# Kernel tuning notes

Measured on AMD Instinct MI355X. Metric: run time of the kernel, lower is better.

Reference implementation:

```python
import jax, jax.numpy as jnp
import numpy as np

B, H, N, D, R, HIDDEN = 4, 12, 1025, 64, 1, 32


def _make_tables(N, R):
    # Geometry tables, mirroring FlexAttentionCPB.init_tables
    P = N - R
    S = int(P ** 0.5)
    assert S * S == P
    rng = np.arange(-(S - 1), S, dtype=np.float32)        # [2S-1]
    dY, dX = np.meshgrid(rng, rng, indexing='ij')
    rel = np.stack([dY / max(S - 1, 1), dX / max(S - 1, 1)], axis=-1).reshape(-1, 2)
    rel_table = np.sign(rel) * np.log1p(np.abs(rel))      # [(2S-1)^2, 2]
    yy = np.arange(S)
    Y, X = np.meshgrid(yy, yy, indexing='ij')
    flat = np.stack([Y, X], 0).reshape(2, -1)             # [2, P]
    d = (flat[:, :, None] - flat[:, None, :]).transpose(1, 2, 0).copy()  # [P,P,2]
    d[:, :, 0] += S - 1
    d[:, :, 1] += S - 1
    d[:, :, 0] *= 2 * S - 1
    l_idx = d.sum(-1).astype(np.int32)
    idx = np.full((N, N), -1, dtype=np.int32)
    idx[R:, R:] = l_idx
    return jnp.asarray(rel_table, jnp.float32), jnp.asarray(idx)


def setup_inputs() -> dict:
    key = jax.random.key(0)
    ks = jax.random.split(key, 8)
    rel_table, idx_table = _make_tables(N, R)
    return {
        'q': jax.random.normal(ks[0], (B, H, N, D), jnp.float32),
        'k': jax.random.normal(ks[1], (B, H, N, D), jnp.float32),
        'v': jax.random.normal(ks[2], (B, H, N, D), jnp.float32),
        'mu': jax.random.normal(ks[3], (B, H, 2, N), jnp.float32),
        'w1': jax.random.normal(ks[4], (2, HIDDEN), jnp.float32) * 0.5,
        'b1': jax.random.normal(ks[5], (HIDDEN,), jnp.float32) * 0.05,
        'w2': jax.random.normal(ks[6], (HIDDEN, H), jnp.float32) * 0.1,
        'gamma': jnp.zeros((H,), jnp.float32),   # nn.Parameter(torch.zeros(H))
        'rel_table': rel_table,
        'idx_table': idx_table,
    }


def reference(q, k, v, mu, w1, b1, w2, gamma, rel_table, idx_table):
    d = q.shape[-1]
    # CPB MLP: Linear(2,hidden)+GELU(exact)+Linear(hidden,H,no bias) -> [L,H]
    bt = jax.nn.gelu(rel_table @ w1 + b1, approximate=False) @ w2
    has_bias = (idx_table >= 0)                       # [N,N] == (q>=R)&(kv>=R)
    idx_c = jnp.where(has_bias, idx_table, 0)
    bias = jnp.transpose(bt[idx_c], (2, 0, 1))        # [H,N,N]
    mu_q = mu[:, :, 0, :]                             # [B,H,N]
    mu_k = mu[:, :, 1, :]
    gate = jax.nn.sigmoid(gamma)[None, :, None, None] * (
        mu_q[..., :, None] + mu_k[..., None, :])      # [B,H,N,N]
    scale = 1.0 / jnp.sqrt(jnp.asarray(d, q.dtype))
    scores = jnp.einsum('bhqd,bhkd->bhqk', q, k) * scale
    scores = scores + has_bias[None, None].astype(scores.dtype) * gate * bias[None]
    attn = jax.nn.softmax(scores, axis=-1)
    return jnp.einsum('bhqk,bhkd->bhqd', attn, v)
```

## Files before the change

kernel.cpp:

```cpp
#include <hip/hip_runtime.h>
#include <math.h>

#define B_ 4
#define H_ 12
#define N_ 1025
#define D_ 64
#define HID_ 32
#define TBL_ 3969
#define NQT 17
#define NBLK (B_ * H_ * NQT)
#define LOG2E 1.44269504f
#define THR_ 12.0f

typedef _Float16 half8 __attribute__((ext_vector_type(8)));
typedef __fp16 fp16x2 __attribute__((ext_vector_type(2)));
typedef float f32x4 __attribute__((ext_vector_type(4)));
typedef float f32x4u __attribute__((ext_vector_type(4), aligned(4)));

#if defined(__has_builtin)
#if __has_builtin(__builtin_amdgcn_exp2f)
#define EX2 __builtin_amdgcn_exp2f
#else
#define EX2 exp2f
#endif
#else
#define EX2 exp2f
#endif

#define AKT_OFF 0
#define BTR_OFF 208896
#define KF_OFF 399408
#define VF_OFF 7084080

__device__ __forceinline__ void stage16(const _Float16* gsrc, _Float16* ldst) {
    __builtin_amdgcn_global_load_lds(
        (const __attribute__((address_space(1))) void*)gsrc,
        (__attribute__((address_space(3))) void*)ldst, 16, 0, 0);
}

__global__ __launch_bounds__(256) void prep(
    const float* __restrict__ K, const float* __restrict__ V,
    const float* __restrict__ MU, const float* __restrict__ GAMMA,
    const float* __restrict__ rel, const float* __restrict__ w1,
    const float* __restrict__ b1, const float* __restrict__ w2,
    _Float16* __restrict__ Kf, _Float16* __restrict__ Vf,
    float* __restrict__ akT, float* __restrict__ btR) {
    const int bid = blockIdx.x;
    const int tid = threadIdx.x;
    if (bid < NBLK) {
        __shared__ float Vls[64 * 65];
        __shared__ __align__(16) float Kls[64 * 64];
        const int bh = bid / NQT, kt = bid % NQT;
        const size_t base = (size_t)bh * (N_ * D_);
        const int k0 = kt * 64;
#pragma unroll
        for (int it = 0; it < 4; ++it) {
            const int idx = it * 256 + tid;
            const int kr = idx >> 4, c4 = (idx & 15) << 2;
            const int kg = k0 + kr;
            float4 v4 = make_float4(0, 0, 0, 0), k4 = v4;
            if (kg < N_) {
                v4 = *(const float4*)(V + base + (size_t)kg * D_ + c4);
                k4 = *(const float4*)(K + base + (size_t)kg * D_ + c4);
            }
            Vls[(c4 + 0) * 65 + kr] = v4.x;
            Vls[(c4 + 1) * 65 + kr] = v4.y;
            Vls[(c4 + 2) * 65 + kr] = v4.z;
            Vls[(c4 + 3) * 65 + kr] = v4.w;
            const int gi = (c4 >> 2) ^ (kr & 15);
            *(float4*)&Kls[kr * 64 + (gi << 2)] = k4;
        }
        if (tid < 64) {
            const int kk = k0 + tid;
            const int h = bh % H_;
            const float sgl = LOG2E / (1.f + __expf(-GAMMA[h]));
            float a = 0.f;
            if (kk >= 1 && kk < N_) a = sgl * MU[((size_t)bh * 2 + 1) * N_ + kk];
            akT[bh * 1088 + kk] = a;
        }
        __syncthreads();
        const int lane = tid & 63, lq = lane & 15, g = lane >> 4;
        const int fbh = tid >> 6;
        const size_t tb = (size_t)(bh * NQT + kt) * 4096;
#pragma unroll
        for (int x = 0; x < 2; ++x) {
            const int fb = fbh + x * 4;
            {
                const int kh = fb >> 2, dg = fb & 3;
                const float* vp = &Vls[(dg * 16 + lq) * 65 + kh * 32 + g * 8];
                half8 v8;
#pragma unroll
                for (int j = 0; j < 8; ++j) v8[j] = (_Float16)vp[j];
                *(half8*)&Vf[tb + fb * 512 + lane * 8] = v8;
            }
            {
                const int row = (fb >> 1) * 16 + lq;
                const int col = (fb & 1) * 32 + g * 8;
                const int ga = ((col >> 2) + 0) ^ (row & 15);
                const int gb = ((col >> 2) + 1) ^ (row & 15);
                f32x4 a = *(const f32x4*)&Kls[row * 64 + (ga << 2)];
                f32x4 b = *(const f32x4*)&Kls[row * 64 + (gb << 2)];
                half8 k8;
                k8[0] = (_Float16)a[0]; k8[1] = (_Float16)a[1];
                k8[2] = (_Float16)a[2]; k8[3] = (_Float16)a[3];
                k8[4] = (_Float16)b[0]; k8[5] = (_Float16)b[1];
                k8[6] = (_Float16)b[2]; k8[7] = (_Float16)b[3];
                *(half8*)&Kf[tb + fb * 512 + lane * 8] = k8;
            }
        }
    } else {
        const int i = (bid - NBLK) * 256 + tid;
        if (i < TBL_) {
            const float x0 = rel[2 * i + 0], x1 = rel[2 * i + 1];
            float acc[H_];
#pragma unroll
            for (int h = 0; h < H_; ++h) acc[h] = 0.f;
#pragma unroll
            for (int j = 0; j < HID_; ++j) {
                float t = fmaf(x0, w1[j], fmaf(x1, w1[HID_ + j], b1[j]));
                float gl = 0.5f * t * (1.f + erff(t * 0.7071067811865475f));
#pragma unroll
                for (int h = 0; h < H_; ++h) acc[h] = fmaf(gl, w2[j * H_ + h], acc[h]);
            }
#pragma unroll
            for (int h = 0; h < H_; ++h) btR[h * TBL_ + (TBL_ - 1 - i)] = acc[h];
        }
    }
}

__global__ __launch_bounds__(256, 4) void flex_attn(
    const float* __restrict__ Q, const _Float16* __restrict__ Kf,
    const _Float16* __restrict__ Vf, const float* __restrict__ MU,
    const float* __restrict__ GAMMA, const char* __restrict__ btb,
    const float* __restrict__ akT, float* __restrict__ OUT) {
    __shared__ __align__(16) _Float16 Ks[2][4096];
    __shared__ __align__(16) _Float16 Vs[2][4096];

    const int bid = blockIdx.x;
    const int swz0 = (bid & 7) * (NBLK / 8) + (bid >> 3);
    const int bh = swz0 / NQT;
    const int qt = swz0 % NQT;
    const int h = bh % H_;
    const int tid = threadIdx.x;
    const int w = tid >> 6;
    const int lane = tid & 63;
    const int lq = lane & 15;
    const int g = lane >> 4;

    const size_t base = (size_t)bh * (N_ * D_);
    const float sg = LOG2E / (1.f + __expf(-GAMMA[h]));

    const int qrow = qt * 64 + w * 16 + lq;
    const bool qv = qrow < N_;

    half8 qf[2];
#pragma unroll
    for (int dh = 0; dh < 2; ++dh) {
        float4 t0 = make_float4(0, 0, 0, 0), t1 = t0;
        if (qv) {
            const float4* qp = (const float4*)(Q + base + (size_t)qrow * D_ + dh * 32 + g * 8);
            t0 = qp[0]; t1 = qp[1];
        }
        const float qs = 0.125f * LOG2E;
        half8 q8;
        q8[0] = (_Float16)(t0.x * qs); q8[1] = (_Float16)(t0.y * qs);
        q8[2] = (_Float16)(t0.z * qs); q8[3] = (_Float16)(t0.w * qs);
        q8[4] = (_Float16)(t1.x * qs); q8[5] = (_Float16)(t1.y * qs);
        q8[6] = (_Float16)(t1.z * qs); q8[7] = (_Float16)(t1.w * qs);
        qf[dh] = q8;
    }

    const bool qb = qv && (qrow >= 1);
    const float qbf = qb ? 1.f : 0.f;
    float aq = 0.f;
    int cq = 0;
    if (qb) {
        const int pq = qrow - 1;
        cq = (pq >> 5) * 63 + (pq & 31);
        aq = sg * MU[(size_t)bh * 2 * N_ + qrow];
    }
    int boff4[4];
#pragma unroll
    for (int kg = 0; kg < 4; ++kg) {
        const int pk0 = kg * 16 + g * 4 - 1;
        const int ck0 = (pk0 >> 5) * 63 + (pk0 & 31);
        boff4[kg] = (h * TBL_ + 1984 - cq + ck0) * 4;
    }
    const float* akb = akT + bh * 1088;
    const _Float16* kfb = Kf + (size_t)bh * NQT * 4096;
    const _Float16* vfb = Vf + (size_t)bh * NQT * 4096;

    f32x4 o[4];
    const f32x4 zz = {0.f, 0.f, 0.f, 0.f};
#pragma unroll
    for (int dg = 0; dg < 4; ++dg) o[dg] = zz;
    float m = 0.f, lsum = 0.f;

    stage16(kfb + (2 * w + 0) * 512 + lane * 8, &Ks[0][(2 * w + 0) * 512]);
    stage16(kfb + (2 * w + 1) * 512 + lane * 8, &Ks[0][(2 * w + 1) * 512]);
    stage16(vfb + (2 * w + 0) * 512 + lane * 8, &Vs[0][(2 * w + 0) * 512]);
    stage16(vfb + (2 * w + 1) * 512 + lane * 8, &Vs[0][(2 * w + 1) * 512]);
    __syncthreads();

    const int pswz = (lq & 7) << 4;

    for (int t = 0; t < NQT; ++t) {
        const int buf = t & 1;
        const int kt0 = t * 64;
        char* plw = (char*)&Ks[buf][0] + w * 2048;

        float bt16[16];
#pragma unroll
        for (int kg = 0; kg < 4; ++kg) {
            const int off = boff4[kg];
            if (kg & 1) {
                f32x4u f4 = *(const f32x4u*)(btb + off);
                bt16[kg * 4 + 0] = f4[0];
                bt16[kg * 4 + 1] = f4[1];
                bt16[kg * 4 + 2] = f4[2];
                bt16[kg * 4 + 3] = f4[3];
            } else {
                const bool cross = (g == 0);
                f32x4u f4 = *(const f32x4u*)(btb + off + (cross ? 128 : 0));
                const float s0v = *(const float*)(btb + off);
                bt16[kg * 4 + 0] = s0v;
                bt16[kg * 4 + 1] = cross ? f4[0] : f4[1];
                bt16[kg * 4 + 2] = cross ? f4[1] : f4[2];
                bt16[kg * 4 + 3] = cross ? f4[2] : f4[3];
            }
            boff4[kg] += 504;
        }
        f32x4 akq[4];
#pragma unroll
        for (int kg = 0; kg < 4; ++kg)
            akq[kg] = *(const f32x4*)(akb + kt0 + kg * 16 + g * 4);

        if (t + 1 < NQT) {
            const _Float16* kn = kfb + (size_t)(t + 1) * 4096;
            const _Float16* vn = vfb + (size_t)(t + 1) * 4096;
            stage16(kn + (2 * w + 0) * 512 + lane * 8, &Ks[buf ^ 1][(2 * w + 0) * 512]);
            stage16(kn + (2 * w + 1) * 512 + lane * 8, &Ks[buf ^ 1][(2 * w + 1) * 512]);
            stage16(vn + (2 * w + 0) * 512 + lane * 8, &Vs[buf ^ 1][(2 * w + 0) * 512]);
            stage16(vn + (2 * w + 1) * 512 + lane * 8, &Vs[buf ^ 1][(2 * w + 1) * 512]);
        }

        const _Float16* ksl = &Ks[buf][lane * 8];
        f32x4 sa[4];
#pragma unroll
        for (int kg = 0; kg < 4; ++kg) {
            half8 a0 = *(const half8*)(ksl + (2 * kg + 0) * 512);
            half8 a1 = *(const half8*)(ksl + (2 * kg + 1) * 512);
            f32x4 z = zz;
            z = __builtin_amdgcn_mfma_f32_16x16x32_f16(a0, qf[0], z, 0, 0, 0);
            z = __builtin_amdgcn_mfma_f32_16x16x32_f16(a1, qf[1], z, 0, 0, 0);
            sa[kg] = z;
        }
        asm volatile("s_waitcnt lgkmcnt(0)" ::: "memory");
        __builtin_amdgcn_s_barrier();
        __builtin_amdgcn_sched_barrier(0);

        if (t == 0 && g == 0) bt16[0] = 0.f;
        float s[16];
#pragma unroll
        for (int kg = 0; kg < 4; ++kg) {
#pragma unroll
            for (int r = 0; r < 4; ++r) {
                const int i = kg * 4 + r;
                s[i] = fmaf(fmaf(qbf, akq[kg][r], aq), bt16[i], sa[kg][r]);
            }
        }
        if (t == NQT - 1) {
#pragma unroll
            for (int kg = 0; kg < 4; ++kg)
#pragma unroll
                for (int r = 0; r < 4; ++r) {
                    const int i = kg * 4 + r;
                    if (1024 + kg * 16 + g * 4 + r >= N_) s[i] = -1e30f;
                }
        }

        float lmax = s[0];
#pragma unroll
        for (int i = 1; i < 16; ++i) lmax = fmaxf(lmax, s[i]);
        if (t == 0) {
            float mt = fmaxf(lmax, __shfl_xor(lmax, 16));
            m = fmaxf(mt, __shfl_xor(mt, 32));
        } else if (!__all(lmax <= m + THR_)) {
            float mt = fmaxf(lmax, __shfl_xor(lmax, 16));
            mt = fmaxf(mt, __shfl_xor(mt, 32));
            const float mnew = fmaxf(m, mt);
            const float cc = EX2(m - mnew);
            m = mnew;
            lsum *= cc;
            float cc4[4];
#pragma unroll
            for (int r = 0; r < 4; ++r) cc4[r] = __shfl(cc, g * 4 + r);
#pragma unroll
            for (int dg = 0; dg < 4; ++dg)
#pragma unroll
                for (int r = 0; r < 4; ++r) o[dg][r] *= cc4[r];
        }
        float pv16[16];
        float ls0 = 0.f, ls1 = 0.f;
#pragma unroll
        for (int i = 0; i < 16; i += 2) {
            pv16[i] = EX2(s[i] - m);
            pv16[i + 1] = EX2(s[i + 1] - m);
            ls0 += pv16[i];
            ls1 += pv16[i + 1];
        }
        lsum += ls0 + ls1;

#pragma unroll
        for (int kg = 0; kg < 4; ++kg) {
            fp16x2 h0 = __builtin_amdgcn_cvt_pkrtz(pv16[kg * 4 + 0], pv16[kg * 4 + 1]);
            fp16x2 h1 = __builtin_amdgcn_cvt_pkrtz(pv16[kg * 4 + 2], pv16[kg * 4 + 3]);
            uint2 u = make_uint2(__builtin_bit_cast(uint32_t, h0),
                                 __builtin_bit_cast(uint32_t, h1));
            *(uint2*)(plw + lq * 128 + ((kg * 32 + g * 8) ^ pswz)) = u;
        }

#pragma unroll
        for (int kh = 0; kh < 2; ++kh) {
            half8 pa = *(const half8*)(plw + lq * 128 + ((kh * 64 + g * 16) ^ pswz));
#pragma unroll
            for (int dg = 0; dg < 4; ++dg) {
                half8 vb8 = *(const half8*)&Vs[buf][(kh * 4 + dg) * 512 + lane * 8];
                o[dg] = __builtin_amdgcn_mfma_f32_16x16x32_f16(pa, vb8, o[dg], 0, 0, 0);
            }
        }
        __syncthreads();
    }

    lsum += __shfl_xor(lsum, 16);
    lsum += __shfl_xor(lsum, 32);
    const float linv = 1.f / lsum;
    float li4[4];
#pragma unroll
    for (int r = 0; r < 4; ++r) li4[r] = __shfl(linv, g * 4 + r);
#pragma unroll
    for (int dg = 0; dg < 4; ++dg) {
#pragma unroll
        for (int r = 0; r < 4; ++r) {
            const int qq = qt * 64 + w * 16 + g * 4 + r;
            if (qq < N_) OUT[base + (size_t)qq * D_ + dg * 16 + lq] = o[dg][r] * li4[r];
        }
    }
}

extern "C" void kernel_launch(void* const* d_in, const int* in_sizes, int n_in,
                              void* d_out, int out_size, void* d_ws, size_t ws_size,
                              hipStream_t stream) {
    const float* q = (const float*)d_in[0];
    const float* k = (const float*)d_in[1];
    const float* v = (const float*)d_in[2];
    const float* mu = (const float*)d_in[3];
    const float* w1 = (const float*)d_in[4];
    const float* b1 = (const float*)d_in[5];
    const float* w2 = (const float*)d_in[6];
    const float* gamma = (const float*)d_in[7];
    const float* rel = (const float*)d_in[8];

    char* ws = (char*)d_ws;
    float* akT = (float*)(ws + AKT_OFF);
    float* btR = (float*)(ws + BTR_OFF);
    _Float16* Kf = (_Float16*)(ws + KF_OFF);
    _Float16* Vf = (_Float16*)(ws + VF_OFF);

    prep<<<NBLK + (TBL_ + 255) / 256, 256, 0, stream>>>(k, v, mu, gamma, rel, w1, b1, w2,
                                                        Kf, Vf, akT, btR);
    flex_attn<<<NBLK, 256, 0, stream>>>(q, Kf, Vf, mu, gamma, ws + BTR_OFF, akT,
                                        (float*)d_out);
}
```

Measured before the change: 61.41 us.

## Split KV range across two blocks per query tile with merge kernel

```diff
diff --git a/kernel.cpp b/kernel.cpp
--- a/kernel.cpp
+++ b/kernel.cpp
@@ -9,6 +9,7 @@
 #define TBL_ 3969
 #define NQT 17
 #define NBLK (B_ * H_ * NQT)
+#define NBLK2 (NBLK * 2)
 #define LOG2E 1.44269504f
 #define THR_ 12.0f
 
@@ -31,6 +32,9 @@
 #define BTR_OFF 208896
 #define KF_OFF 399408
 #define VF_OFF 7084080
+#define OP_OFF 13768768
+#define ML_OFF 27138112
+#define WS_NEED 27973696ull
 
 __device__ __forceinline__ void stage16(const _Float16* gsrc, _Float16* ldst) {
     __builtin_amdgcn_global_load_lds(
@@ -128,18 +132,34 @@
     }
 }
 
+template <int SPLIT>
 __global__ __launch_bounds__(256, 4) void flex_attn(
     const float* __restrict__ Q, const _Float16* __restrict__ Kf,
     const _Float16* __restrict__ Vf, const float* __restrict__ MU,
     const float* __restrict__ GAMMA, const char* __restrict__ btb,
-    const float* __restrict__ akT, float* __restrict__ OUT) {
+    const float* __restrict__ akT, _Float16* __restrict__ Opart,
+    float* __restrict__ mlb, float* __restrict__ OUT) {
     __shared__ __align__(16) _Float16 Ks[2][4096];
     __shared__ __align__(16) _Float16 Vs[2][4096];
 
     const int bid = blockIdx.x;
-    const int swz0 = (bid & 7) * (NBLK / 8) + (bid >> 3);
-    const int bh = swz0 / NQT;
-    const int qt = swz0 % NQT;
+    int bh, qt, kh, tstart, tend;
+    if (SPLIT) {
+        const int swz0 = (bid & 7) * (NBLK2 / 8) + (bid >> 3);
+        bh = swz0 / (NQT * 2);
+        const int rr = swz0 % (NQT * 2);
+        qt = rr >> 1;
+        kh = rr & 1;
+        tstart = kh ? 9 : 0;
+        tend = kh ? NQT : 9;
+    } else {
+        const int swz0 = (bid & 7) * (NBLK / 8) + (bid >> 3);
+        bh = swz0 / NQT;
+        qt = swz0 % NQT;
+        kh = 0;
+        tstart = 0;
+        tend = NQT;
+    }
     const int h = bh % H_;
     const int tid = threadIdx.x;
     const int w = tid >> 6;
@@ -184,7 +204,7 @@
     for (int kg = 0; kg < 4; ++kg) {
         const int pk0 = kg * 16 + g * 4 - 1;
         const int ck0 = (pk0 >> 5) * 63 + (pk0 & 31);
-        boff4[kg] = (h * TBL_ + 1984 - cq + ck0) * 4;
+        boff4[kg] = (h * TBL_ + 1984 - cq + ck0) * 4 + tstart * 504;
     }
     const float* akb = akT + bh * 1088;
     const _Float16* kfb = Kf + (size_t)bh * NQT * 4096;
@@ -196,15 +216,21 @@
     for (int dg = 0; dg < 4; ++dg) o[dg] = zz;
     float m = 0.f, lsum = 0.f;
 
-    stage16(kfb + (2 * w + 0) * 512 + lane * 8, &Ks[0][(2 * w + 0) * 512]);
-    stage16(kfb + (2 * w + 1) * 512 + lane * 8, &Ks[0][(2 * w + 1) * 512]);
-    stage16(vfb + (2 * w + 0) * 512 + lane * 8, &Vs[0][(2 * w + 0) * 512]);
-    stage16(vfb + (2 * w + 1) * 512 + lane * 8, &Vs[0][(2 * w + 1) * 512]);
+    {
+        const _Float16* kp = kfb + (size_t)tstart * 4096;
+        const _Float16* vp = vfb + (size_t)tstart * 4096;
+        _Float16* kd = &Ks[tstart & 1][0];
+        _Float16* vd = &Vs[tstart & 1][0];
+        stage16(kp + (2 * w + 0) * 512 + lane * 8, kd + (2 * w + 0) * 512);
+        stage16(kp + (2 * w + 1) * 512 + lane * 8, kd + (2 * w + 1) * 512);
+        stage16(vp + (2 * w + 0) * 512 + lane * 8, vd + (2 * w + 0) * 512);
+        stage16(vp + (2 * w + 1) * 512 + lane * 8, vd + (2 * w + 1) * 512);
+    }
     __syncthreads();
 
     const int pswz = (lq & 7) << 4;
 
-    for (int t = 0; t < NQT; ++t) {
+    for (int t = tstart; t < tend; ++t) {
         const int buf = t & 1;
         const int kt0 = t * 64;
         char* plw = (char*)&Ks[buf][0] + w * 2048;
@@ -235,7 +261,7 @@
         for (int kg = 0; kg < 4; ++kg)
             akq[kg] = *(const f32x4*)(akb + kt0 + kg * 16 + g * 4);
 
-        if (t + 1 < NQT) {
+        if (t + 1 < tend) {
             const _Float16* kn = kfb + (size_t)(t + 1) * 4096;
             const _Float16* vn = vfb + (size_t)(t + 1) * 4096;
             stage16(kn + (2 * w + 0) * 512 + lane * 8, &Ks[buf ^ 1][(2 * w + 0) * 512]);
@@ -282,7 +308,7 @@
         float lmax = s[0];
 #pragma unroll
         for (int i = 1; i < 16; ++i) lmax = fmaxf(lmax, s[i]);
-        if (t == 0) {
+        if (t == tstart) {
             float mt = fmaxf(lmax, __shfl_xor(lmax, 16));
             m = fmaxf(mt, __shfl_xor(mt, 32));
         } else if (!__all(lmax <= m + THR_)) {
@@ -321,11 +347,11 @@
         }
 
 #pragma unroll
-        for (int kh = 0; kh < 2; ++kh) {
-            half8 pa = *(const half8*)(plw + lq * 128 + ((kh * 64 + g * 16) ^ pswz));
+        for (int khx = 0; khx < 2; ++khx) {
+            half8 pa = *(const half8*)(plw + lq * 128 + ((khx * 64 + g * 16) ^ pswz));
 #pragma unroll
             for (int dg = 0; dg < 4; ++dg) {
-                half8 vb8 = *(const half8*)&Vs[buf][(kh * 4 + dg) * 512 + lane * 8];
+                half8 vb8 = *(const half8*)&Vs[buf][(khx * 4 + dg) * 512 + lane * 8];
                 o[dg] = __builtin_amdgcn_mfma_f32_16x16x32_f16(pa, vb8, o[dg], 0, 0, 0);
             }
         }
@@ -338,14 +364,64 @@
     float li4[4];
 #pragma unroll
     for (int r = 0; r < 4; ++r) li4[r] = __shfl(linv, g * 4 + r);
-#pragma unroll
-    for (int dg = 0; dg < 4; ++dg) {
-#pragma unroll
-        for (int r = 0; r < 4; ++r) {
-            const int qq = qt * 64 + w * 16 + g * 4 + r;
-            if (qq < N_) OUT[base + (size_t)qq * D_ + dg * 16 + lq] = o[dg][r] * li4[r];
-        }
-    }
+    if (SPLIT) {
+        _Float16* op = Opart + (size_t)(bh * 2 + kh) * (1088 * 64);
+#pragma unroll
+        for (int dg = 0; dg < 4; ++dg) {
+#pragma unroll
+            for (int r = 0; r < 4; ++r) {
+                const int qq = qt * 64 + w * 16 + g * 4 + r;
+                op[(size_t)qq * 64 + dg * 16 + lq] = (_Float16)(o[dg][r] * li4[r]);
+            }
+        }
+        if (g == 0 && qv) {
+            float2* mlp = (float2*)mlb + (size_t)(bh * 2 + kh) * 1088 + qrow;
+            *mlp = make_float2(m, lsum);
+        }
+    } else {
+#pragma unroll
+        for (int dg = 0; dg < 4; ++dg) {
+#pragma unroll
+            for (int r = 0; r < 4; ++r) {
+                const int qq = qt * 64 + w * 16 + g * 4 + r;
+                if (qq < N_) OUT[base + (size_t)qq * D_ + dg * 16 + lq] = o[dg][r] * li4[r];
+            }
+        }
+    }
+}
+
+__global__ __launch_bounds__(256) void merge(const _Float16* __restrict__ Opart,
+                                             const float* __restrict__ mlb,
+                                             float* __restrict__ OUT) {
+    const int idx = blockIdx.x * 256 + threadIdx.x;
+    if (idx >= B_ * H_ * N_ * 8) return;
+    const int d8 = (idx & 7) * 8;
+    const int rg = idx >> 3;
+    const int bh = rg / N_;
+    const int qq = rg % N_;
+    const float2 ml0 = ((const float2*)mlb)[(size_t)(bh * 2 + 0) * 1088 + qq];
+    const float2 ml1 = ((const float2*)mlb)[(size_t)(bh * 2 + 1) * 1088 + qq];
+    const float M = fmaxf(ml0.x, ml1.x);
+    const float w0 = ml0.y * EX2(ml0.x - M);
+    const float w1 = ml1.y * EX2(ml1.x - M);
+    const float inv = 1.f / (w0 + w1);
+    const float c0 = w0 * inv, c1 = w1 * inv;
+    const half8 o0 = *(const half8*)(Opart + (size_t)(bh * 2 + 0) * (1088 * 64) +
+                                     (size_t)qq * 64 + d8);
+    const half8 o1 = *(const half8*)(Opart + (size_t)(bh * 2 + 1) * (1088 * 64) +
+                                     (size_t)qq * 64 + d8);
+    float* op = OUT + (size_t)bh * (N_ * D_) + (size_t)qq * 64 + d8;
+    float4 r0, r1;
+    r0.x = fmaf(c0, (float)o0[0], c1 * (float)o1[0]);
+    r0.y = fmaf(c0, (float)o0[1], c1 * (float)o1[1]);
+    r0.z = fmaf(c0, (float)o0[2], c1 * (float)o1[2]);
+    r0.w = fmaf(c0, (float)o0[3], c1 * (float)o1[3]);
+    r1.x = fmaf(c0, (float)o0[4], c1 * (float)o1[4]);
+    r1.y = fmaf(c0, (float)o0[5], c1 * (float)o1[5]);
+    r1.z = fmaf(c0, (float)o0[6], c1 * (float)o1[6]);
+    r1.w = fmaf(c0, (float)o0[7], c1 * (float)o1[7]);
+    ((float4*)op)[0] = r0;
+    ((float4*)op)[1] = r1;
 }
 
 extern "C" void kernel_launch(void* const* d_in, const int* in_sizes, int n_in,
@@ -366,9 +442,18 @@
     float* btR = (float*)(ws + BTR_OFF);
     _Float16* Kf = (_Float16*)(ws + KF_OFF);
     _Float16* Vf = (_Float16*)(ws + VF_OFF);
+    _Float16* Opart = (_Float16*)(ws + OP_OFF);
+    float* mlb = (float*)(ws + ML_OFF);
 
     prep<<<NBLK + (TBL_ + 255) / 256, 256, 0, stream>>>(k, v, mu, gamma, rel, w1, b1, w2,
                                                         Kf, Vf, akT, btR);
-    flex_attn<<<NBLK, 256, 0, stream>>>(q, Kf, Vf, mu, gamma, ws + BTR_OFF, akT,
-                                        (float*)d_out);
+    if (ws_size >= WS_NEED) {
+        flex_attn<1><<<NBLK2, 256, 0, stream>>>(q, Kf, Vf, mu, gamma, ws + BTR_OFF, akT,
+                                                Opart, mlb, (float*)d_out);
+        merge<<<(B_ * H_ * N_ * 8 + 255) / 256, 256, 0, stream>>>(Opart, mlb,
+                                                                  (float*)d_out);
+    } else {
+        flex_attn<0><<<NBLK, 256, 0, stream>>>(q, Kf, Vf, mu, gamma, ws + BTR_OFF, akT,
+                                               Opart, mlb, (float*)d_out);
+    }
 }
```

New measurement: 65.50 us. 6.6% more time.

## Split KV tile across warp pairs, each warp handling two query groups with LDS merge

Applied to the files above, without the earlier changes.

```diff
diff --git a/kernel.cpp b/kernel.cpp
--- a/kernel.cpp
+++ b/kernel.cpp
@@ -128,7 +128,7 @@
     }
 }
 
-__global__ __launch_bounds__(256, 4) void flex_attn(
+__global__ __launch_bounds__(256, 3) void flex_attn(
     const float* __restrict__ Q, const _Float16* __restrict__ Kf,
     const _Float16* __restrict__ Vf, const float* __restrict__ MU,
     const float* __restrict__ GAMMA, const char* __restrict__ btb,
@@ -143,6 +143,8 @@
     const int h = bh % H_;
     const int tid = threadIdx.x;
     const int w = tid >> 6;
+    const int kh = w & 1;
+    const int qh = w >> 1;
     const int lane = tid & 63;
     const int lq = lane & 15;
     const int g = lane >> 4;
@@ -150,51 +152,61 @@
     const size_t base = (size_t)bh * (N_ * D_);
     const float sg = LOG2E / (1.f + __expf(-GAMMA[h]));
 
-    const int qrow = qt * 64 + w * 16 + lq;
-    const bool qv = qrow < N_;
-
-    half8 qf[2];
-#pragma unroll
-    for (int dh = 0; dh < 2; ++dh) {
-        float4 t0 = make_float4(0, 0, 0, 0), t1 = t0;
-        if (qv) {
-            const float4* qp = (const float4*)(Q + base + (size_t)qrow * D_ + dh * 32 + g * 8);
-            t0 = qp[0]; t1 = qp[1];
-        }
-        const float qs = 0.125f * LOG2E;
-        half8 q8;
-        q8[0] = (_Float16)(t0.x * qs); q8[1] = (_Float16)(t0.y * qs);
-        q8[2] = (_Float16)(t0.z * qs); q8[3] = (_Float16)(t0.w * qs);
-        q8[4] = (_Float16)(t1.x * qs); q8[5] = (_Float16)(t1.y * qs);
-        q8[6] = (_Float16)(t1.z * qs); q8[7] = (_Float16)(t1.w * qs);
-        qf[dh] = q8;
-    }
-
-    const bool qb = qv && (qrow >= 1);
-    const float qbf = qb ? 1.f : 0.f;
-    float aq = 0.f;
-    int cq = 0;
-    if (qb) {
-        const int pq = qrow - 1;
-        cq = (pq >> 5) * 63 + (pq & 31);
-        aq = sg * MU[(size_t)bh * 2 * N_ + qrow];
-    }
-    int boff4[4];
-#pragma unroll
-    for (int kg = 0; kg < 4; ++kg) {
-        const int pk0 = kg * 16 + g * 4 - 1;
-        const int ck0 = (pk0 >> 5) * 63 + (pk0 & 31);
-        boff4[kg] = (h * TBL_ + 1984 - cq + ck0) * 4;
+    half8 qf[2][2];
+    bool qb[2];
+    float aq[2], qbf[2];
+    int cq[2];
+#pragma unroll
+    for (int qg = 0; qg < 2; ++qg) {
+        const int qrow = qt * 64 + qh * 32 + qg * 16 + lq;
+        const bool qv = qrow < N_;
+#pragma unroll
+        for (int dh = 0; dh < 2; ++dh) {
+            float4 t0 = make_float4(0, 0, 0, 0), t1 = t0;
+            if (qv) {
+                const float4* qp =
+                    (const float4*)(Q + base + (size_t)qrow * D_ + dh * 32 + g * 8);
+                t0 = qp[0]; t1 = qp[1];
+            }
+            const float qs = 0.125f * LOG2E;
+            half8 q8;
+            q8[0] = (_Float16)(t0.x * qs); q8[1] = (_Float16)(t0.y * qs);
+            q8[2] = (_Float16)(t0.z * qs); q8[3] = (_Float16)(t0.w * qs);
+            q8[4] = (_Float16)(t1.x * qs); q8[5] = (_Float16)(t1.y * qs);
+            q8[6] = (_Float16)(t1.z * qs); q8[7] = (_Float16)(t1.w * qs);
+            qf[qg][dh] = q8;
+        }
+        qb[qg] = qv && (qrow >= 1);
+        qbf[qg] = qb[qg] ? 1.f : 0.f;
+        aq[qg] = 0.f;
+        cq[qg] = 0;
+        if (qb[qg]) {
+            const int pq = qrow - 1;
+            cq[qg] = (pq >> 5) * 63 + (pq & 31);
+            aq[qg] = sg * MU[(size_t)bh * 2 * N_ + qrow];
+        }
+    }
+    int boff4[2][2];
+#pragma unroll
+    for (int qg = 0; qg < 2; ++qg) {
+#pragma unroll
+        for (int kg = 0; kg < 2; ++kg) {
+            const int pk0 = kh * 32 + kg * 16 + g * 4 - 1;
+            const int ck0 = (pk0 >> 5) * 63 + (pk0 & 31);
+            boff4[qg][kg] = (h * TBL_ + 1984 - cq[qg] + ck0) * 4;
+        }
     }
     const float* akb = akT + bh * 1088;
     const _Float16* kfb = Kf + (size_t)bh * NQT * 4096;
     const _Float16* vfb = Vf + (size_t)bh * NQT * 4096;
 
-    f32x4 o[4];
+    f32x4 o[2][4];
     const f32x4 zz = {0.f, 0.f, 0.f, 0.f};
 #pragma unroll
-    for (int dg = 0; dg < 4; ++dg) o[dg] = zz;
-    float m = 0.f, lsum = 0.f;
+    for (int qg = 0; qg < 2; ++qg)
+#pragma unroll
+        for (int dg = 0; dg < 4; ++dg) o[qg][dg] = zz;
+    float m[2] = {0.f, 0.f}, lsum[2] = {0.f, 0.f};
 
     stage16(kfb + (2 * w + 0) * 512 + lane * 8, &Ks[0][(2 * w + 0) * 512]);
     stage16(kfb + (2 * w + 1) * 512 + lane * 8, &Ks[0][(2 * w + 1) * 512]);
@@ -202,38 +214,39 @@
     stage16(vfb + (2 * w + 1) * 512 + lane * 8, &Vs[0][(2 * w + 1) * 512]);
     __syncthreads();
 
-    const int pswz = (lq & 7) << 4;
+    const int pswz = (lq & 3) << 4;
 
     for (int t = 0; t < NQT; ++t) {
         const int buf = t & 1;
         const int kt0 = t * 64;
         char* plw = (char*)&Ks[buf][0] + w * 2048;
 
-        float bt16[16];
-#pragma unroll
-        for (int kg = 0; kg < 4; ++kg) {
-            const int off = boff4[kg];
-            if (kg & 1) {
-                f32x4u f4 = *(const f32x4u*)(btb + off);
-                bt16[kg * 4 + 0] = f4[0];
-                bt16[kg * 4 + 1] = f4[1];
-                bt16[kg * 4 + 2] = f4[2];
-                bt16[kg * 4 + 3] = f4[3];
-            } else {
-                const bool cross = (g == 0);
-                f32x4u f4 = *(const f32x4u*)(btb + off + (cross ? 128 : 0));
-                const float s0v = *(const float*)(btb + off);
-                bt16[kg * 4 + 0] = s0v;
-                bt16[kg * 4 + 1] = cross ? f4[0] : f4[1];
-                bt16[kg * 4 + 2] = cross ? f4[1] : f4[2];
-                bt16[kg * 4 + 3] = cross ? f4[2] : f4[3];
-            }
-            boff4[kg] += 504;
-        }
-        f32x4 akq[4];
-#pragma unroll
-        for (int kg = 0; kg < 4; ++kg)
-            akq[kg] = *(const f32x4*)(akb + kt0 + kg * 16 + g * 4);
+        float bt[2][8];
+#pragma unroll
+        for (int qg = 0; qg < 2; ++qg) {
+#pragma unroll
+            for (int kg = 0; kg < 2; ++kg) {
+                const int off = boff4[qg][kg];
+                if (kg == 1) {
+                    f32x4u f4 = *(const f32x4u*)(btb + off);
+                    bt[qg][4] = f4[0]; bt[qg][5] = f4[1];
+                    bt[qg][6] = f4[2]; bt[qg][7] = f4[3];
+                } else {
+                    const bool cross = (g == 0);
+                    f32x4u f4 = *(const f32x4u*)(btb + off + (cross ? 128 : 0));
+                    const float s0v = *(const float*)(btb + off);
+                    bt[qg][0] = s0v;
+                    bt[qg][1] = cross ? f4[0] : f4[1];
+                    bt[qg][2] = cross ? f4[1] : f4[2];
+                    bt[qg][3] = cross ? f4[2] : f4[3];
+                }
+                boff4[qg][kg] += 504;
+            }
+        }
+        f32x4 akq[2];
+#pragma unroll
+        for (int kg = 0; kg < 2; ++kg)
+            akq[kg] = *(const f32x4*)(akb + kt0 + kh * 32 + kg * 16 + g * 4);
 
         if (t + 1 < NQT) {
             const _Float16* kn = kfb + (size_t)(t + 1) * 4096;
@@ -244,106 +257,146 @@
             stage16(vn + (2 * w + 1) * 512 + lane * 8, &Vs[buf ^ 1][(2 * w + 1) * 512]);
         }
 
-        const _Float16* ksl = &Ks[buf][lane * 8];
-        f32x4 sa[4];
-#pragma unroll
-        for (int kg = 0; kg < 4; ++kg) {
+        const _Float16* ksl = &Ks[buf][kh * 2048 + lane * 8];
+        f32x4 sa[2][2];
+#pragma unroll
+        for (int kg = 0; kg < 2; ++kg) {
             half8 a0 = *(const half8*)(ksl + (2 * kg + 0) * 512);
             half8 a1 = *(const half8*)(ksl + (2 * kg + 1) * 512);
-            f32x4 z = zz;
-            z = __builtin_amdgcn_mfma_f32_16x16x32_f16(a0, qf[0], z, 0, 0, 0);
-            z = __builtin_amdgcn_mfma_f32_16x16x32_f16(a1, qf[1], z, 0, 0, 0);
-            sa[kg] = z;
+#pragma unroll
+            for (int qg = 0; qg < 2; ++qg) {
+                f32x4 z = zz;
+                z = __builtin_amdgcn_mfma_f32_16x16x32_f16(a0, qf[qg][0], z, 0, 0, 0);
+                z = __builtin_amdgcn_mfma_f32_16x16x32_f16(a1, qf[qg][1], z, 0, 0, 0);
+                sa[qg][kg] = z;
+            }
         }
         asm volatile("s_waitcnt lgkmcnt(0)" ::: "memory");
         __builtin_amdgcn_s_barrier();
         __builtin_amdgcn_sched_barrier(0);
 
-        if (t == 0 && g == 0) bt16[0] = 0.f;
-        float s[16];
-#pragma unroll
-        for (int kg = 0; kg < 4; ++kg) {
-#pragma unroll
-            for (int r = 0; r < 4; ++r) {
-                const int i = kg * 4 + r;
-                s[i] = fmaf(fmaf(qbf, akq[kg][r], aq), bt16[i], sa[kg][r]);
-            }
-        }
-        if (t == NQT - 1) {
-#pragma unroll
-            for (int kg = 0; kg < 4; ++kg)
+        if (t == 0 && kh == 0 && g == 0) { bt[0][0] = 0.f; bt[1][0] = 0.f; }
+#pragma unroll
+        for (int qg = 0; qg < 2; ++qg) {
+            float s[8];
+#pragma unroll
+            for (int kg = 0; kg < 2; ++kg)
 #pragma unroll
                 for (int r = 0; r < 4; ++r) {
                     const int i = kg * 4 + r;
-                    if (1024 + kg * 16 + g * 4 + r >= N_) s[i] = -1e30f;
+                    s[i] = fmaf(fmaf(qbf[qg], akq[kg][r], aq[qg]), bt[qg][i],
+                                sa[qg][kg][r]);
                 }
-        }
-
-        float lmax = s[0];
-#pragma unroll
-        for (int i = 1; i < 16; ++i) lmax = fmaxf(lmax, s[i]);
-        if (t == 0) {
-            float mt = fmaxf(lmax, __shfl_xor(lmax, 16));
-            m = fmaxf(mt, __shfl_xor(mt, 32));
-        } else if (!__all(lmax <= m + THR_)) {
-            float mt = fmaxf(lmax, __shfl_xor(lmax, 16));
-            mt = fmaxf(mt, __shfl_xor(mt, 32));
-            const float mnew = fmaxf(m, mt);
-            const float cc = EX2(m - mnew);
-            m = mnew;
-            lsum *= cc;
-            float cc4[4];
-#pragma unroll
-            for (int r = 0; r < 4; ++r) cc4[r] = __shfl(cc, g * 4 + r);
+            if (t == NQT - 1) {
+#pragma unroll
+                for (int kg = 0; kg < 2; ++kg)
+#pragma unroll
+                    for (int r = 0; r < 4; ++r) {
+                        const bool keep = (kh == 0) && (kg == 0) && (g == 0) && (r == 0);
+                        if (!keep) s[kg * 4 + r] = -1e30f;
+                    }
+            }
+            float lmax = s[0];
+#pragma unroll
+            for (int i = 1; i < 8; ++i) lmax = fmaxf(lmax, s[i]);
+            if (t == 0) {
+                float mt = fmaxf(lmax, __shfl_xor(lmax, 16));
+                m[qg] = fmaxf(mt, __shfl_xor(mt, 32));
+            } else if (!__all(lmax <= m[qg] + THR_)) {
+                float mt = fmaxf(lmax, __shfl_xor(lmax, 16));
+                mt = fmaxf(mt, __shfl_xor(mt, 32));
+                const float mnew = fmaxf(m[qg], mt);
+                const float cc = EX2(m[qg] - mnew);
+                m[qg] = mnew;
+                lsum[qg] *= cc;
+                float cc4[4];
+#pragma unroll
+                for (int r = 0; r < 4; ++r) cc4[r] = __shfl(cc, g * 4 + r);
+#pragma unroll
+                for (int dg = 0; dg < 4; ++dg)
+#pragma unroll
+                    for (int r = 0; r < 4; ++r) o[qg][dg][r] *= cc4[r];
+            }
+            float pv[8];
+            float ls0 = 0.f, ls1 = 0.f;
+#pragma unroll
+            for (int i = 0; i < 8; i += 2) {
+                pv[i] = EX2(s[i] - m[qg]);
+                pv[i + 1] = EX2(s[i + 1] - m[qg]);
+                ls0 += pv[i];
+                ls1 += pv[i + 1];
+            }
+            lsum[qg] += ls0 + ls1;
+#pragma unroll
+            for (int kg = 0; kg < 2; ++kg) {
+                fp16x2 h0 = __builtin_amdgcn_cvt_pkrtz(pv[kg * 4 + 0], pv[kg * 4 + 1]);
+                fp16x2 h1 = __builtin_amdgcn_cvt_pkrtz(pv[kg * 4 + 2], pv[kg * 4 + 3]);
+                uint2 u = make_uint2(__builtin_bit_cast(uint32_t, h0),
+                                     __builtin_bit_cast(uint32_t, h1));
+                *(uint2*)(plw + qg * 1024 + lq * 64 + ((kg * 32 + g * 8) ^ pswz)) = u;
+            }
+        }
+
+#pragma unroll
+        for (int dg = 0; dg < 4; ++dg) {
+            half8 vb8 = *(const half8*)&Vs[buf][(kh * 4 + dg) * 512 + lane * 8];
+#pragma unroll
+            for (int qg = 0; qg < 2; ++qg) {
+                half8 pa = *(const half8*)(plw + qg * 1024 + lq * 64 + ((g * 16) ^ pswz));
+                o[qg][dg] = __builtin_amdgcn_mfma_f32_16x16x32_f16(pa, vb8, o[qg][dg],
+                                                                   0, 0, 0);
+            }
+        }
+        __syncthreads();
+    }
+
+#pragma unroll
+    for (int qg = 0; qg < 2; ++qg) {
+        lsum[qg] += __shfl_xor(lsum[qg], 16);
+        lsum[qg] += __shfl_xor(lsum[qg], 32);
+    }
+    float* oxch = (float*)&Ks[0][0];
+    float* mlx = (float*)&Vs[0][0];
+    if (kh == 1) {
+#pragma unroll
+        for (int qg = 0; qg < 2; ++qg) {
 #pragma unroll
             for (int dg = 0; dg < 4; ++dg)
 #pragma unroll
-                for (int r = 0; r < 4; ++r) o[dg][r] *= cc4[r];
-        }
-        float pv16[16];
-        float ls0 = 0.f, ls1 = 0.f;
-#pragma unroll
-        for (int i = 0; i < 16; i += 2) {
-            pv16[i] = EX2(s[i] - m);
-            pv16[i + 1] = EX2(s[i + 1] - m);
-            ls0 += pv16[i];
-            ls1 += pv16[i + 1];
-        }
-        lsum += ls0 + ls1;
-
-#pragma unroll
-        for (int kg = 0; kg < 4; ++kg) {
-            fp16x2 h0 = __builtin_amdgcn_cvt_pkrtz(pv16[kg * 4 + 0], pv16[kg * 4 + 1]);
-            fp16x2 h1 = __builtin_amdgcn_cvt_pkrtz(pv16[kg * 4 + 2], pv16[kg * 4 + 3]);
-            uint2 u = make_uint2(__builtin_bit_cast(uint32_t, h0),
-                                 __builtin_bit_cast(uint32_t, h1));
-            *(uint2*)(plw + lq * 128 + ((kg * 32 + g * 8) ^ pswz)) = u;
-        }
-
-#pragma unroll
-        for (int kh = 0; kh < 2; ++kh) {
-            half8 pa = *(const half8*)(plw + lq * 128 + ((kh * 64 + g * 16) ^ pswz));
+                for (int r = 0; r < 4; ++r)
+                    oxch[qh * 2048 + (qg * 16 + g * 4 + r) * 64 + dg * 16 + lq] =
+                        o[qg][dg][r];
+            if (g == 0) {
+                mlx[qh * 64 + qg * 16 + lq] = m[qg];
+                mlx[128 + qh * 64 + qg * 16 + lq] = lsum[qg];
+            }
+        }
+    }
+    __syncthreads();
+    if (kh == 0) {
+#pragma unroll
+        for (int qg = 0; qg < 2; ++qg) {
+            const float m1 = mlx[qh * 64 + qg * 16 + lq];
+            const float l1 = mlx[128 + qh * 64 + qg * 16 + lq];
+            const float M = fmaxf(m[qg], m1);
+            const float w0 = EX2(m[qg] - M), w1 = EX2(m1 - M);
+            const float inv = 1.f / fmaf(lsum[qg], w0, l1 * w1);
+            const float f0 = w0 * inv, f1 = w1 * inv;
 #pragma unroll
             for (int dg = 0; dg < 4; ++dg) {
-                half8 vb8 = *(const half8*)&Vs[buf][(kh * 4 + dg) * 512 + lane * 8];
-                o[dg] = __builtin_amdgcn_mfma_f32_16x16x32_f16(pa, vb8, o[dg], 0, 0, 0);
-            }
-        }
-        __syncthreads();
-    }
-
-    lsum += __shfl_xor(lsum, 16);
-    lsum += __shfl_xor(lsum, 32);
-    const float linv = 1.f / lsum;
-    float li4[4];
-#pragma unroll
-    for (int r = 0; r < 4; ++r) li4[r] = __shfl(linv, g * 4 + r);
-#pragma unroll
-    for (int dg = 0; dg < 4; ++dg) {
-#pragma unroll
-        for (int r = 0; r < 4; ++r) {
-            const int qq = qt * 64 + w * 16 + g * 4 + r;
-            if (qq < N_) OUT[base + (size_t)qq * D_ + dg * 16 + lq] = o[dg][r] * li4[r];
+#pragma unroll
+                for (int r = 0; r < 4; ++r) {
+                    const int ql = qg * 16 + g * 4 + r;
+                    const int qq = qt * 64 + qh * 32 + ql;
+                    if (qq < N_) {
+                        const float f0r = __shfl(f0, g * 4 + r);
+                        const float f1r = __shfl(f1, g * 4 + r);
+                        OUT[base + (size_t)qq * D_ + dg * 16 + lq] =
+                            fmaf(f0r, o[qg][dg][r],
+                                 f1r * oxch[qh * 2048 + ql * 64 + dg * 16 + lq]);
+                    }
+                }
+            }
         }
     }
 }
```

Result: slower. 72.14 us (+17.5%).
